# Performance work log

Measured on AMD Instinct MI355X. Metric: run time of the kernel, lower is better.

## Reference

```python
import jax, jax.numpy as jnp
import numpy as np

M, N, D, L, DEPTH, WIDTH, BATCH = 64, 4096, 64, 32, 4, 256, 1024
WIN = 2 * L + 1


def setup_inputs() -> dict:
    key = jax.random.key(0)
    ks = jax.random.split(key, 5)
    u = jax.random.normal(ks[0], (BATCH, D), dtype=jnp.float32)
    # xavier-style scaled gaussians for weights, zeros for biases (matches torch init pattern)
    weight0 = jax.random.normal(ks[1], (M, WIDTH, D), dtype=jnp.float32) * (2.0 / (WIDTH + D)) ** 0.5
    bias0 = jnp.zeros((M, WIDTH, 1), dtype=jnp.float32)
    weight = jax.random.normal(ks[2], (DEPTH - 1, M, WIDTH, WIDTH), dtype=jnp.float32) * (1.0 / WIDTH) ** 0.5
    bias = jnp.zeros((DEPTH - 1, M, WIDTH, 1), dtype=jnp.float32)
    weight_final = jax.random.normal(ks[3], (M, WIN, WIDTH), dtype=jnp.float32) * (2.0 / (WIN + WIDTH)) ** 0.5
    bias_final = jnp.zeros((M, WIN, 1), dtype=jnp.float32)
    xi = jax.random.normal(ks[4], (M, N + 2 * L), dtype=jnp.float32) * (2.0 / (M + N + 2 * L)) ** 0.5
    return {"u": u, "weight0": weight0, "bias0": bias0, "weight": weight,
            "bias": bias, "weight_final": weight_final, "bias_final": bias_final, "xi": xi}


def reference(u, weight0, bias0, weight, bias, weight_final, bias_final, xi) -> jnp.ndarray:
    act = jax.nn.sigmoid
    # per-M shared MLP: u1 [M, width, batch]
    u1 = act(jnp.einsum('mwd,bd->mwb', weight0, u) + bias0)
    for i in range(weight.shape[0]):  # small fixed depth loop
        u1 = act(jnp.einsum('mwv,mvb->mwb', weight[i], u1) + bias[i])
    G = act(jnp.einsum('mjw,mwb->mjb', weight_final, u1) + bias_final)
    # sliding-window correlation: out[n, b] = sum_{m,j} xi[m, n+j] * G[m, j, b]
    win = G.shape[1]
    n_out = xi.shape[1] - (win - 1)
    idx = jnp.arange(n_out)[:, None] + jnp.arange(win)[None, :]
    xw = xi[:, idx]
    return jnp.einsum('mnj,mjb->nb', xw, G)  # [N, batch]
```

## Files before the change

kernel.cpp:

```cpp
#include <hip/hip_runtime.h>
#include <math.h>

typedef __attribute__((ext_vector_type(8))) short short8;
typedef __attribute__((ext_vector_type(4))) float floatx4;
typedef __attribute__((ext_vector_type(4))) unsigned short ushort4v;

__device__ __forceinline__ void load_lds16(const void* g, void* l) {
    __builtin_amdgcn_global_load_lds((const __attribute__((address_space(1))) void*)g,
                                     (__attribute__((address_space(3))) void*)l,
                                     16, 0, 0);
}

__device__ __forceinline__ unsigned short f2bf(float x) {
    union { float f; unsigned int u; } v; v.f = x;
    unsigned int r = v.u + 0x7fffu + ((v.u >> 16) & 1u);
    return (unsigned short)(r >> 16);
}

__device__ __forceinline__ unsigned int pack_bf(float f0, float f1) {
    union { float f; unsigned int u; } a, b;
    a.f = f0; b.f = f1;
    return __builtin_amdgcn_perm(b.u + 0x8000u, a.u + 0x8000u, 0x07060302u);
}

__device__ __forceinline__ float fast_exp2(float x) {
#if __has_builtin(__builtin_amdgcn_exp2f)
    return __builtin_amdgcn_exp2f(x);
#else
    return __expf(x * 0.69314718056f);
#endif
}

__device__ __forceinline__ float fast_rcp(float x) {
#if __has_builtin(__builtin_amdgcn_rcpf)
    return __builtin_amdgcn_rcpf(x);
#else
    return 1.0f / x;
#endif
}

#define NEG_LOG2E (-1.4426950408889634f)

__device__ __forceinline__ float sigm(float x) { return 1.0f / (1.0f + __expf(-x)); }

__global__ void prep(const float* __restrict__ w0, const float* __restrict__ w,
                     const float* __restrict__ wf, const float* __restrict__ xi,
                     unsigned short* __restrict__ w0d, unsigned short* __restrict__ wd,
                     unsigned short* __restrict__ wfd, unsigned int* __restrict__ xw) {
    const int bid = blockIdx.x;
    if (bid < 6656) {
        const bool is0 = bid < 512;
        const int c = (is0 ? bid : bid - 512) * 256 + threadIdx.x;
        const int cpm = is0 ? 2048 : 8192;
        const int Kk  = is0 ? 2 : 8;
        const int K   = Kk * 32;
        const int mm  = c / cpm;
        const int cm  = c - mm * cpm;
        const int rblk = cm / (Kk * 64);
        const int rem  = cm - rblk * (Kk * 64);
        const int kk   = rem >> 6;
        const int lane = rem & 63;
        const int r  = rblk * 16 + (lane & 15);
        const int k0 = kk * 32 + (lane >> 4) * 8;
        const float* srcp = (is0 ? w0 : w) + ((size_t)mm * 256 + r) * K + k0;
        unsigned short* dstp = (is0 ? w0d : wd) + (size_t)c * 8;
        float4 a = *(const float4*)srcp;
        float4 b = *(const float4*)(srcp + 4);
        short8 o = { (short)f2bf(a.x), (short)f2bf(a.y), (short)f2bf(a.z), (short)f2bf(a.w),
                     (short)f2bf(b.x), (short)f2bf(b.y), (short)f2bf(b.z), (short)f2bf(b.w) };
        *(short8*)dstp = o;
    } else if (bid < 7680) {
        const int c = (bid - 6656) * 256 + threadIdx.x;
        const int m  = c >> 12;
        const int cm = c & 4095;
        const int rblk = cm >> 9;
        const int rem  = cm & 511;
        const int kk   = rem >> 6;
        const int lane = rem & 63;
        const int r  = rblk * 16 + (lane & 15);
        const int k0 = kk * 32 + (lane >> 4) * 8;
        short8 o = {0,0,0,0,0,0,0,0};
        if (r < 65) {
            const float* srcp = wf + ((size_t)m * 65 + r) * 256 + k0;
            float4 a = *(const float4*)srcp;
            float4 b = *(const float4*)(srcp + 4);
            o = (short8){ (short)f2bf(a.x), (short)f2bf(a.y), (short)f2bf(a.z), (short)f2bf(a.w),
                          (short)f2bf(b.x), (short)f2bf(b.y), (short)f2bf(b.z), (short)f2bf(b.w) };
        }
        *(short8*)(wfd + (size_t)c * 8) = o;
    } else {
        const int n = bid - 7680;
        #pragma unroll
        for (int t = 0; t < 9; ++t) {
            const int idx = t * 256 + threadIdx.x;
            if (idx < 2176) {
                const int m = idx / 34;
                const int pos = idx - m * 34;
                const int j0 = pos * 2;
                const float* xim = xi + (size_t)m * 4160 + n;
                const float v0 = (j0 < 65) ? xim[j0] : 0.0f;
                const float v1 = (j0 + 1 < 65) ? xim[j0 + 1] : 0.0f;
                xw[(size_t)n * 2176 + idx] =
                    (unsigned int)f2bf(v0) | ((unsigned int)f2bf(v1) << 16);
            }
        }
    }
}

template<int K, int I>
__device__ __forceinline__ void mlp_mfma(
    const unsigned short* __restrict__ Wt, const unsigned short* src,
    int wave, int lane, floatx4 (*acc)[4])
{
    constexpr int Kk = K / 32;
    const int quad = lane >> 4, l16 = lane & 15;
    const int rblk0 = wave * I;
    const floatx4 zero = {0.f, 0.f, 0.f, 0.f};
    #pragma unroll
    for (int i = 0; i < I; ++i)
        #pragma unroll
        for (int j = 0; j < 4; ++j) acc[i][j] = zero;

    const unsigned short* wbase = Wt + (size_t)((rblk0 * Kk) * 64 + lane) * 8;

    short8 a[2][I];
    #pragma unroll
    for (int i = 0; i < I; ++i)
        a[0][i] = *(const short8*)(wbase + (size_t)(i * Kk) * 512);

    #pragma unroll
    for (int kk = 0; kk < Kk; ++kk) {
        const int cur = kk & 1;
        if (kk + 1 < Kk) {
            #pragma unroll
            for (int i = 0; i < I; ++i)
                a[cur ^ 1][i] = *(const short8*)(wbase + (size_t)(i * Kk + kk + 1) * 512);
        }
        short8 bf[4];
        #pragma unroll
        for (int j = 0; j < 4; ++j) {
            const int cb = j * 16 + l16;
            bf[j] = *(const short8*)&src[cb * K + (((kk * 4 + quad) ^ (cb & 7)) * 8)];
        }
        #pragma unroll
        for (int i = 0; i < I; ++i)
            #pragma unroll
            for (int j = 0; j < 4; ++j)
                acc[i][j] = __builtin_amdgcn_mfma_f32_16x16x32_bf16(a[cur][i], bf[j], acc[i][j], 0, 0, 0);
    }
}

__device__ __forceinline__ void mlp_write(
    const float* __restrict__ bm, unsigned short* dst,
    int wave, int lane, floatx4 (*acc)[4])
{
    const int quad = lane >> 4, l16 = lane & 15;
    const int rbw = wave * 64;
    #pragma unroll
    for (int i = 0; i < 4; ++i) {
        const int rb = rbw + i * 16 + quad * 4;
        float c0 = bm[rb]     * NEG_LOG2E;
        float c1 = bm[rb + 1] * NEG_LOG2E;
        float c2 = bm[rb + 2] * NEG_LOG2E;
        float c3 = bm[rb + 3] * NEG_LOG2E;
        #pragma unroll
        for (int j = 0; j < 4; ++j) {
            const int cb = j * 16 + l16;
            float r0 = fast_rcp(1.0f + fast_exp2(fmaf(acc[i][j][0], NEG_LOG2E, c0)));
            float r1 = fast_rcp(1.0f + fast_exp2(fmaf(acc[i][j][1], NEG_LOG2E, c1)));
            float r2 = fast_rcp(1.0f + fast_exp2(fmaf(acc[i][j][2], NEG_LOG2E, c2)));
            float r3 = fast_rcp(1.0f + fast_exp2(fmaf(acc[i][j][3], NEG_LOG2E, c3)));
            uint2 o = { pack_bf(r0, r1), pack_bf(r2, r3) };
            *(uint2*)&dst[cb * 256 + (((rb >> 3) ^ (cb & 7)) * 8) + (rb & 7)] = o;
        }
    }
}

__global__ __launch_bounds__(256, 4)
void fused_mlp(const float* __restrict__ u,
               const unsigned short* __restrict__ w0_bf, const float* __restrict__ b0_,
               const unsigned short* __restrict__ w_bf,  const float* __restrict__ b_,
               const unsigned short* __restrict__ wf_bf, const float* __restrict__ bf_,
               unsigned short* __restrict__ Gflat) {
    __shared__ unsigned short X[64 * 256];

    const int bid = blockIdx.x;
    const int xcd = bid & 7, slot = bid >> 3;
    const int m  = (xcd << 3) + (slot >> 4);
    const int b0 = (slot & 15) << 6;
    const int tid = threadIdx.x, wave = tid >> 6, lane = tid & 63;

    {
        const int b = tid >> 2, dc = tid & 3;
        const float* up = u + (size_t)(b0 + b) * 64 + dc * 16;
        float4 v0 = *(const float4*)(up);
        float4 v1 = *(const float4*)(up + 4);
        float4 v2 = *(const float4*)(up + 8);
        float4 v3 = *(const float4*)(up + 12);
        uint4 p0 = { pack_bf(v0.x, v0.y), pack_bf(v0.z, v0.w),
                     pack_bf(v1.x, v1.y), pack_bf(v1.z, v1.w) };
        uint4 p1 = { pack_bf(v2.x, v2.y), pack_bf(v2.z, v2.w),
                     pack_bf(v3.x, v3.y), pack_bf(v3.z, v3.w) };
        *(uint4*)&X[b * 64 + (((dc * 2)     ^ (b & 7)) * 8)] = p0;
        *(uint4*)&X[b * 64 + (((dc * 2 + 1) ^ (b & 7)) * 8)] = p1;
    }
    __syncthreads();

    floatx4 acc[4][4];

    mlp_mfma<64, 4>(w0_bf + (size_t)m * 16384, X, wave, lane, acc);
    __syncthreads();
    mlp_write(b0_ + (size_t)m * 256, X, wave, lane, acc);
    __syncthreads();

    #pragma unroll 1
    for (int l = 0; l < 3; ++l) {
        mlp_mfma<256, 4>(w_bf + ((size_t)l * 64 + m) * 65536, X, wave, lane, acc);
        __syncthreads();
        mlp_write(b_ + ((size_t)l * 64 + m) * 256, X, wave, lane, acc);
        __syncthreads();
    }

    {
        floatx4 acf[2][4];
        mlp_mfma<256, 2>(wf_bf + (size_t)m * 32768, X, wave, lane, acf);
        const int quad = lane >> 4, l16 = lane & 15;
        const float* bm = bf_ + (size_t)m * 65;
        unsigned short* Gg = Gflat + (size_t)b0 * 4352 + m * 68;
        #pragma unroll
        for (int i = 0; i < 2; ++i) {
            const int rb = wave * 32 + i * 16 + quad * 4;
            if (rb < 68) {
                float c[4];
                #pragma unroll
                for (int rr = 0; rr < 4; ++rr)
                    c[rr] = (rb + rr < 65) ? bm[rb + rr] * NEG_LOG2E : 0.0f;
                #pragma unroll
                for (int j = 0; j < 4; ++j) {
                    const int cb = j * 16 + l16;
                    float r0 = fast_rcp(1.0f + fast_exp2(fmaf(acf[i][j][0], NEG_LOG2E, c[0])));
                    float r1 = fast_rcp(1.0f + fast_exp2(fmaf(acf[i][j][1], NEG_LOG2E, c[1])));
                    float r2 = fast_rcp(1.0f + fast_exp2(fmaf(acf[i][j][2], NEG_LOG2E, c[2])));
                    float r3 = fast_rcp(1.0f + fast_exp2(fmaf(acf[i][j][3], NEG_LOG2E, c[3])));
                    uint2 o = { pack_bf(r0, r1), pack_bf(r2, r3) };
                    *(uint2*)&Gg[(size_t)cb * 4352 + rb] = o;
                }
            }
        }
    }
}

__global__ __launch_bounds__(256, 3)
void contract_gemm(const unsigned short* __restrict__ XW,
                   const unsigned short* __restrict__ G,
                   float* __restrict__ P) {
    const int bid = blockIdx.x;
    const int xcd = bid & 7, slot = bid >> 3;
    const int kc  = slot >> 5;
    const int rst = slot & 31;
    const int r0 = ((xcd << 2) + (rst >> 3)) << 7;
    const int c0 = (rst & 7) << 7;
    const int kb = kc * 1088;
    float* Pc = P + (size_t)kc * 4096 * 1024;

    __shared__ unsigned short As[128 * 64];
    __shared__ unsigned short Bs[128 * 64];

    const int tid = threadIdx.x;
    const int wave = tid >> 6, lane = tid & 63;
    const int quad = lane >> 4, l16 = lane & 15;
    const int wr = (wave & 1) * 64;
    const int wc = (wave >> 1) * 64;
    const int srow = wave * 32 + (lane >> 3);
    const int spos = lane & 7;

    floatx4 acc[4][4];
    const floatx4 zero = {0.f, 0.f, 0.f, 0.f};
    #pragma unroll
    for (int i = 0; i < 4; ++i)
        #pragma unroll
        for (int j = 0; j < 4; ++j) acc[i][j] = zero;

    for (int k0 = kb; k0 < kb + 1088; k0 += 64) {
        #pragma unroll
        for (int t = 0; t < 4; ++t) {
            const int row = srow + t * 8;
            const int fc  = spos ^ (row & 7);
            load_lds16(XW + (size_t)(r0 + row) * 4352 + k0 + fc * 8,
                       &As[(wave * 32 + t * 8) * 64]);
            load_lds16(G + (size_t)(c0 + row) * 4352 + k0 + fc * 8,
                       &Bs[(wave * 32 + t * 8) * 64]);
        }
        __syncthreads();

        #pragma unroll
        for (int kk = 0; kk < 2; ++kk) {
            short8 af[4], bfr[4];
            #pragma unroll
            for (int i = 0; i < 4; ++i) {
                const int ra = wr + i * 16 + l16;
                af[i]  = *(const short8*)&As[ra * 64 + (((kk * 4 + quad) ^ (ra & 7)) * 8)];
                const int cb = wc + i * 16 + l16;
                bfr[i] = *(const short8*)&Bs[cb * 64 + (((kk * 4 + quad) ^ (cb & 7)) * 8)];
            }
            #pragma unroll
            for (int i = 0; i < 4; ++i)
                #pragma unroll
                for (int j = 0; j < 4; ++j)
                    acc[i][j] = __builtin_amdgcn_mfma_f32_16x16x32_bf16(af[i], bfr[j], acc[i][j], 0, 0, 0);
        }
        __syncthreads();
    }

    #pragma unroll
    for (int i = 0; i < 4; ++i) {
        const int rb = r0 + wr + i * 16 + quad * 4;
        #pragma unroll
        for (int rr = 0; rr < 4; ++rr)
            #pragma unroll
            for (int j = 0; j < 4; ++j) {
                const int col = c0 + wc + j * 16 + l16;
                Pc[(size_t)(rb + rr) * 1024 + col] = acc[i][j][rr];
            }
    }
}

__global__ void reduce4(const float* __restrict__ P, float* __restrict__ out) {
    const int i = blockIdx.x * 256 + threadIdx.x;
    const float4* p = (const float4*)P;
    float4 a = p[i], b = p[i + 1048576], c = p[i + 2097152], d = p[i + 3145728];
    ((float4*)out)[i] = (float4){ a.x + b.x + c.x + d.x, a.y + b.y + c.y + d.y,
                                  a.z + b.z + c.z + d.z, a.w + b.w + c.w + d.w };
}

extern "C" void kernel_launch(void* const* d_in, const int* in_sizes, int n_in,
                              void* d_out, int out_size, void* d_ws, size_t ws_size,
                              hipStream_t stream) {
    const float* u   = (const float*)d_in[0];
    const float* w0  = (const float*)d_in[1];
    const float* b0_ = (const float*)d_in[2];
    const float* w   = (const float*)d_in[3];
    const float* b   = (const float*)d_in[4];
    const float* wf  = (const float*)d_in[5];
    const float* bf_ = (const float*)d_in[6];
    const float* xi  = (const float*)d_in[7];
    float* out = (float*)d_out;

    unsigned short* w0_bf = (unsigned short*)d_ws;
    unsigned short* w_bf  = w0_bf + 1048576;
    unsigned short* wf_bf = w_bf  + 12582912;
    unsigned short* Gflat = wf_bf + 2097152;
    unsigned short* XW    = Gflat + 4456448;
    float*          P     = (float*)(XW + 17825792);

    prep<<<11776, 256, 0, stream>>>(w0, w, wf, xi, w0_bf, w_bf, wf_bf, (unsigned int*)XW);
    fused_mlp<<<1024, 256, 0, stream>>>(u, w0_bf, b0_, w_bf, b, wf_bf, bf_, Gflat);
    contract_gemm<<<1024, 256, 0, stream>>>(XW, Gflat, P);
    reduce4<<<4096, 256, 0, stream>>>(P, out);
}
```

Before: 231.7 us.

## Double batch tile per MLP block and keep layer weights resident in registers

The fused MLP kernel now handles 128 batch columns per block instead of 64, which halves the grid to 512 blocks and doubles shared memory for activations. Each layer's weight fragments are loaded into registers once and reused across two 64-column sub-tiles, so global weight traffic per batch element is halved. The cost is heavy register pressure (a 4x8 short8 weight array plus accumulators), which drops launch bounds to 2 blocks per SM and removes the double-buffered weight prefetch. It also adds barriers between sub-tiles.

```diff
diff --git a/kernel.cpp b/kernel.cpp
--- a/kernel.cpp
+++ b/kernel.cpp
@@ -3,7 +3,6 @@
 
 typedef __attribute__((ext_vector_type(8))) short short8;
 typedef __attribute__((ext_vector_type(4))) float floatx4;
-typedef __attribute__((ext_vector_type(4))) unsigned short ushort4v;
 
 __device__ __forceinline__ void load_lds16(const void* g, void* l) {
     __builtin_amdgcn_global_load_lds((const __attribute__((address_space(1))) void*)g,
@@ -40,8 +39,6 @@
 }
 
 #define NEG_LOG2E (-1.4426950408889634f)
-
-__device__ __forceinline__ float sigm(float x) { return 1.0f / (1.0f + __expf(-x)); }
 
 __global__ void prep(const float* __restrict__ w0, const float* __restrict__ w,
                      const float* __restrict__ wf, const float* __restrict__ xi,
@@ -108,56 +105,52 @@
 }
 
 template<int K, int I>
-__device__ __forceinline__ void mlp_mfma(
-    const unsigned short* __restrict__ Wt, const unsigned short* src,
-    int wave, int lane, floatx4 (*acc)[4])
+__device__ __forceinline__ void load_w(
+    const unsigned short* __restrict__ Wt, int wave, int lane, short8 (&w)[I][K / 32])
 {
     constexpr int Kk = K / 32;
-    const int quad = lane >> 4, l16 = lane & 15;
-    const int rblk0 = wave * I;
-    const floatx4 zero = {0.f, 0.f, 0.f, 0.f};
+    const unsigned short* wb = Wt + ((size_t)(wave * I * Kk) * 64 + lane) * 8;
     #pragma unroll
     for (int i = 0; i < I; ++i)
         #pragma unroll
-        for (int j = 0; j < 4; ++j) acc[i][j] = zero;
-
-    const unsigned short* wbase = Wt + (size_t)((rblk0 * Kk) * 64 + lane) * 8;
-
-    short8 a[2][I];
+        for (int kk = 0; kk < Kk; ++kk)
+            w[i][kk] = *(const short8*)(wb + (size_t)(i * Kk + kk) * 512);
+}
+
+template<int K, int I>
+__device__ __forceinline__ void mfma_tile(
+    const short8 (&w)[I][K / 32], const unsigned short* src, int t,
+    int quad, int l16, floatx4 (&acc)[I][4])
+{
+    constexpr int Kk = K / 32;
     #pragma unroll
     for (int i = 0; i < I; ++i)
-        a[0][i] = *(const short8*)(wbase + (size_t)(i * Kk) * 512);
-
+        #pragma unroll
+        for (int j = 0; j < 4; ++j) acc[i][j] = (floatx4){0.f, 0.f, 0.f, 0.f};
     #pragma unroll
     for (int kk = 0; kk < Kk; ++kk) {
-        const int cur = kk & 1;
-        if (kk + 1 < Kk) {
-            #pragma unroll
-            for (int i = 0; i < I; ++i)
-                a[cur ^ 1][i] = *(const short8*)(wbase + (size_t)(i * Kk + kk + 1) * 512);
-        }
         short8 bf[4];
         #pragma unroll
         for (int j = 0; j < 4; ++j) {
-            const int cb = j * 16 + l16;
+            const int cb = t * 64 + j * 16 + l16;
             bf[j] = *(const short8*)&src[cb * K + (((kk * 4 + quad) ^ (cb & 7)) * 8)];
         }
         #pragma unroll
         for (int i = 0; i < I; ++i)
             #pragma unroll
             for (int j = 0; j < 4; ++j)
-                acc[i][j] = __builtin_amdgcn_mfma_f32_16x16x32_bf16(a[cur][i], bf[j], acc[i][j], 0, 0, 0);
-    }
-}
-
-__device__ __forceinline__ void mlp_write(
-    const float* __restrict__ bm, unsigned short* dst,
-    int wave, int lane, floatx4 (*acc)[4])
+                acc[i][j] = __builtin_amdgcn_mfma_f32_16x16x32_bf16(w[i][kk], bf[j], acc[i][j], 0, 0, 0);
+    }
+}
+
+template<int I>
+__device__ __forceinline__ void mlp_write_t(
+    const float* __restrict__ bm, unsigned short* dst, int t,
+    int wave, int quad, int l16, floatx4 (&acc)[I][4])
 {
-    const int quad = lane >> 4, l16 = lane & 15;
-    const int rbw = wave * 64;
-    #pragma unroll
-    for (int i = 0; i < 4; ++i) {
+    const int rbw = wave * (I * 16);
+    #pragma unroll
+    for (int i = 0; i < I; ++i) {
         const int rb = rbw + i * 16 + quad * 4;
         float c0 = bm[rb]     * NEG_LOG2E;
         float c1 = bm[rb + 1] * NEG_LOG2E;
@@ -165,7 +158,7 @@
         float c3 = bm[rb + 3] * NEG_LOG2E;
         #pragma unroll
         for (int j = 0; j < 4; ++j) {
-            const int cb = j * 16 + l16;
+            const int cb = t * 64 + j * 16 + l16;
             float r0 = fast_rcp(1.0f + fast_exp2(fmaf(acc[i][j][0], NEG_LOG2E, c0)));
             float r1 = fast_rcp(1.0f + fast_exp2(fmaf(acc[i][j][1], NEG_LOG2E, c1)));
             float r2 = fast_rcp(1.0f + fast_exp2(fmaf(acc[i][j][2], NEG_LOG2E, c2)));
@@ -176,74 +169,90 @@
     }
 }
 
-__global__ __launch_bounds__(256, 4)
+__global__ __launch_bounds__(256, 2)
 void fused_mlp(const float* __restrict__ u,
                const unsigned short* __restrict__ w0_bf, const float* __restrict__ b0_,
                const unsigned short* __restrict__ w_bf,  const float* __restrict__ b_,
                const unsigned short* __restrict__ wf_bf, const float* __restrict__ bf_,
                unsigned short* __restrict__ Gflat) {
-    __shared__ unsigned short X[64 * 256];
+    __shared__ unsigned short X[128 * 256];
 
     const int bid = blockIdx.x;
     const int xcd = bid & 7, slot = bid >> 3;
-    const int m  = (xcd << 3) + (slot >> 4);
-    const int b0 = (slot & 15) << 6;
+    const int m  = (xcd << 3) + (slot >> 3);
+    const int b0 = (slot & 7) << 7;
     const int tid = threadIdx.x, wave = tid >> 6, lane = tid & 63;
+    const int quad = lane >> 4, l16 = lane & 15;
 
     {
-        const int b = tid >> 2, dc = tid & 3;
-        const float* up = u + (size_t)(b0 + b) * 64 + dc * 16;
-        float4 v0 = *(const float4*)(up);
-        float4 v1 = *(const float4*)(up + 4);
-        float4 v2 = *(const float4*)(up + 8);
-        float4 v3 = *(const float4*)(up + 12);
-        uint4 p0 = { pack_bf(v0.x, v0.y), pack_bf(v0.z, v0.w),
-                     pack_bf(v1.x, v1.y), pack_bf(v1.z, v1.w) };
-        uint4 p1 = { pack_bf(v2.x, v2.y), pack_bf(v2.z, v2.w),
-                     pack_bf(v3.x, v3.y), pack_bf(v3.z, v3.w) };
-        *(uint4*)&X[b * 64 + (((dc * 2)     ^ (b & 7)) * 8)] = p0;
-        *(uint4*)&X[b * 64 + (((dc * 2 + 1) ^ (b & 7)) * 8)] = p1;
+        const int b = tid >> 1, hk = tid & 1;
+        const float* up = u + (size_t)(b0 + b) * 64 + hk * 32;
+        #pragma unroll
+        for (int c = 0; c < 4; ++c) {
+            float4 v0 = *(const float4*)(up + c * 8);
+            float4 v1 = *(const float4*)(up + c * 8 + 4);
+            uint4 p = { pack_bf(v0.x, v0.y), pack_bf(v0.z, v0.w),
+                        pack_bf(v1.x, v1.y), pack_bf(v1.z, v1.w) };
+            *(uint4*)&X[b * 64 + (((hk * 4 + c) ^ (b & 7)) * 8)] = p;
+        }
     }
     __syncthreads();
 
     floatx4 acc[4][4];
 
-    mlp_mfma<64, 4>(w0_bf + (size_t)m * 16384, X, wave, lane, acc);
-    __syncthreads();
-    mlp_write(b0_ + (size_t)m * 256, X, wave, lane, acc);
-    __syncthreads();
+    {
+        short8 w0r[4][2];
+        load_w<64, 4>(w0_bf + (size_t)m * 16384, wave, lane, w0r);
+        floatx4 acc2[4][4];
+        mfma_tile<64, 4>(w0r, X, 0, quad, l16, acc);
+        mfma_tile<64, 4>(w0r, X, 1, quad, l16, acc2);
+        __syncthreads();
+        mlp_write_t<4>(b0_ + (size_t)m * 256, X, 0, wave, quad, l16, acc);
+        mlp_write_t<4>(b0_ + (size_t)m * 256, X, 1, wave, quad, l16, acc2);
+        __syncthreads();
+    }
 
     #pragma unroll 1
     for (int l = 0; l < 3; ++l) {
-        mlp_mfma<256, 4>(w_bf + ((size_t)l * 64 + m) * 65536, X, wave, lane, acc);
-        __syncthreads();
-        mlp_write(b_ + ((size_t)l * 64 + m) * 256, X, wave, lane, acc);
-        __syncthreads();
-    }
+        short8 wr[4][8];
+        load_w<256, 4>(w_bf + ((size_t)l * 64 + m) * 65536, wave, lane, wr);
+        const float* bm = b_ + ((size_t)l * 64 + m) * 256;
+        mfma_tile<256, 4>(wr, X, 0, quad, l16, acc);
+        __syncthreads();
+        mlp_write_t<4>(bm, X, 0, wave, quad, l16, acc);
+        mfma_tile<256, 4>(wr, X, 1, quad, l16, acc);
+        __syncthreads();
+        mlp_write_t<4>(bm, X, 1, wave, quad, l16, acc);
+    }
+    __syncthreads();
 
     {
-        floatx4 acf[2][4];
-        mlp_mfma<256, 2>(wf_bf + (size_t)m * 32768, X, wave, lane, acf);
-        const int quad = lane >> 4, l16 = lane & 15;
+        short8 wfr[2][8];
+        load_w<256, 2>(wf_bf + (size_t)m * 32768, wave, lane, wfr);
         const float* bm = bf_ + (size_t)m * 65;
         unsigned short* Gg = Gflat + (size_t)b0 * 4352 + m * 68;
-        #pragma unroll
-        for (int i = 0; i < 2; ++i) {
-            const int rb = wave * 32 + i * 16 + quad * 4;
-            if (rb < 68) {
-                float c[4];
-                #pragma unroll
-                for (int rr = 0; rr < 4; ++rr)
-                    c[rr] = (rb + rr < 65) ? bm[rb + rr] * NEG_LOG2E : 0.0f;
-                #pragma unroll
-                for (int j = 0; j < 4; ++j) {
-                    const int cb = j * 16 + l16;
-                    float r0 = fast_rcp(1.0f + fast_exp2(fmaf(acf[i][j][0], NEG_LOG2E, c[0])));
-                    float r1 = fast_rcp(1.0f + fast_exp2(fmaf(acf[i][j][1], NEG_LOG2E, c[1])));
-                    float r2 = fast_rcp(1.0f + fast_exp2(fmaf(acf[i][j][2], NEG_LOG2E, c[2])));
-                    float r3 = fast_rcp(1.0f + fast_exp2(fmaf(acf[i][j][3], NEG_LOG2E, c[3])));
-                    uint2 o = { pack_bf(r0, r1), pack_bf(r2, r3) };
-                    *(uint2*)&Gg[(size_t)cb * 4352 + rb] = o;
+        floatx4 acf[2][4];
+        #pragma unroll
+        for (int t = 0; t < 2; ++t) {
+            mfma_tile<256, 2>(wfr, X, t, quad, l16, acf);
+            #pragma unroll
+            for (int i = 0; i < 2; ++i) {
+                const int rb = wave * 32 + i * 16 + quad * 4;
+                if (rb < 68) {
+                    float c[4];
+                    #pragma unroll
+                    for (int rr = 0; rr < 4; ++rr)
+                        c[rr] = (rb + rr < 65) ? bm[rb + rr] * NEG_LOG2E : 0.0f;
+                    #pragma unroll
+                    for (int j = 0; j < 4; ++j) {
+                        const int cb = t * 64 + j * 16 + l16;
+                        float r0 = fast_rcp(1.0f + fast_exp2(fmaf(acf[i][j][0], NEG_LOG2E, c[0])));
+                        float r1 = fast_rcp(1.0f + fast_exp2(fmaf(acf[i][j][1], NEG_LOG2E, c[1])));
+                        float r2 = fast_rcp(1.0f + fast_exp2(fmaf(acf[i][j][2], NEG_LOG2E, c[2])));
+                        float r3 = fast_rcp(1.0f + fast_exp2(fmaf(acf[i][j][3], NEG_LOG2E, c[3])));
+                        uint2 o = { pack_bf(r0, r1), pack_bf(r2, r3) };
+                        *(uint2*)&Gg[(size_t)cb * 4352 + rb] = o;
+                    }
                 }
             }
         }
@@ -354,7 +363,7 @@
     float*          P     = (float*)(XW + 17825792);
 
     prep<<<11776, 256, 0, stream>>>(w0, w, wf, xi, w0_bf, w_bf, wf_bf, (unsigned int*)XW);
-    fused_mlp<<<1024, 256, 0, stream>>>(u, w0_bf, b0_, w_bf, b, wf_bf, bf_, Gflat);
+    fused_mlp<<<512, 256, 0, stream>>>(u, w0_bf, b0_, w_bf, b, wf_bf, bf_, Gflat);
     contract_gemm<<<1024, 256, 0, stream>>>(XW, Gflat, P);
     reduce4<<<4096, 256, 0, stream>>>(P, out);
 }
```

Measured after the change: 220.4 us. 1.05x faster.
